# Kernel tuning notes

Measured on AMD Instinct MI355X. Metric: run time of the kernel, lower is better.

## Reference

```python
import jax, jax.numpy as jnp
import numpy as np

EPS = 1e-5

@jax.custom_vjp
def round_ste(x):
    return jnp.round(x)

def _round_fwd(x):
    return jnp.round(x), None

def _round_bwd(_, g):
    return (g,)

round_ste.defvjp(_round_fwd, _round_bwd)


def setup_inputs() -> dict:
    key = jax.random.key(0)
    ks = jax.random.split(key, 4)
    x = jax.random.normal(ks[0], (16, 64, 128, 128), dtype=jnp.float32)
    # small init so conv outputs stay in a sane range
    W = jax.random.normal(ks[1], (128, 64, 3, 3), dtype=jnp.float32) * 0.05
    gamma = jnp.ones((128,), dtype=jnp.float32)
    beta = jnp.zeros((128,), dtype=jnp.float32)
    mean = jax.random.normal(ks[2], (128,), dtype=jnp.float32) * 0.1
    var = jax.random.uniform(ks[3], (128,), dtype=jnp.float32) * 0.5 + 0.5
    # Brevitas QuantReLU default learned max ~6.0 (relu6-like init)
    act_scale = jnp.ones((1,), dtype=jnp.float32) * 6.0
    return {"x": x, "W": W, "gamma": gamma, "beta": beta,
            "mean": mean, "var": var, "act_scale": act_scale}


def reference(x, W, gamma, beta, mean, var, act_scale):
    # --- Int8 per-tensor weight quant-dequant (symmetric, scale = maxabs/127) ---
    w_scale = jnp.max(jnp.abs(W)) / 127.0
    qW = jnp.clip(round_ste(W / w_scale), -127.0, 127.0) * w_scale
    # --- conv2d, stride 1, padding 1, no bias (NCHW / OIHW) ---
    y = jax.lax.conv_general_dilated(
        x, qW, window_strides=(1, 1), padding=[(1, 1), (1, 1)],
        dimension_numbers=("NCHW", "OIHW", "NCHW"))
    # --- BatchNorm (inference form with running stats) ---
    scale = (gamma / jnp.sqrt(var + EPS))[None, :, None, None]
    shift = (beta - gamma * mean / jnp.sqrt(var + EPS))[None, :, None, None]
    y = y * scale + shift
    # --- QuantReLU: relu + uint8 per-tensor quant-dequant ---
    y = jax.nn.relu(y)
    s = act_scale[0] / 255.0
    return jnp.clip(round_ste(y / s), 0.0, 255.0) * s
```

## Files before the change

kernel.cpp:

```cpp
#include <hip/hip_runtime.h>
#include <math.h>

typedef __bf16 bf16x8 __attribute__((ext_vector_type(8)));
typedef float  f32x16 __attribute__((ext_vector_type(16)));
typedef float  f32x4v __attribute__((ext_vector_type(4)));

#define CIN    64
#define KOUT   128
#define HGT    128
#define WID    128
#define NBATCH 16
#define BN_EPS 1e-5f

#define WQ_OFF   256u
#define XT_OFF   (1u << 20)
#define WS_NEED  ((size_t)XT_OFF + (size_t)NBATCH * HGT * WID * CIN * 2)

__global__ __launch_bounds__(256) void wmax_kernel(const float* __restrict__ W,
                                                   unsigned* __restrict__ wsmax) {
    int idx = blockIdx.x * 256 + threadIdx.x;
    const float4* W4 = (const float4*)W;
    float4 v = W4[idx];
    float m = fmaxf(fmaxf(fabsf(v.x), fabsf(v.y)), fmaxf(fabsf(v.z), fabsf(v.w)));
    #pragma unroll
    for (int off = 32; off > 0; off >>= 1)
        m = fmaxf(m, __shfl_xor(m, off));
    __shared__ float red[4];
    if ((threadIdx.x & 63) == 0) red[threadIdx.x >> 6] = m;
    __syncthreads();
    if (threadIdx.x == 0) {
        m = fmaxf(fmaxf(red[0], red[1]), fmaxf(red[2], red[3]));
        atomicMax(wsmax, __float_as_uint(m));
    }
}

__global__ __launch_bounds__(256) void pack_w(const float* __restrict__ W,
                                              const unsigned* __restrict__ wsmax,
                                              __bf16* __restrict__ wqp) {
    int bid = blockIdx.x;
    int tap = bid % 9, cs = bid / 9;
    int t = threadIdx.x;
    int lane = t & 63, mf = t >> 6;
    float ws = __uint_as_float(*wsmax) / 127.0f;
    int kout  = mf * 32 + (lane & 31);
    int cbase = cs * 16 + (lane >> 5) * 8;
    bf16x8 o;
    #pragma unroll
    for (int j = 0; j < 8; ++j) {
        float w = W[(size_t)(kout * 64 + cbase + j) * 9 + tap];
        float q = rintf(w / ws);
        q = fminf(fmaxf(q, -127.f), 127.f);
        o[j] = (__bf16)q;
    }
    *(bf16x8*)(wqp + (((size_t)bid * 4 + mf) * 64 + lane) * 8) = o;
}

__global__ __launch_bounds__(256) void xform(const float* __restrict__ x,
                                             __bf16* __restrict__ xT) {
    __shared__ float t[CIN * 32];
    int bid = blockIdx.x;
    int wt = bid & 3;
    int h  = (bid >> 2) & 127;
    int n  = bid >> 9;
    int w0 = wt * 32;
    int tid = threadIdx.x;
    const float* src = x + ((size_t)n * CIN * HGT + h) * WID + w0;
    int wlane = tid & 31;
    int cbase = tid >> 5;
    #pragma unroll
    for (int it = 0; it < 8; ++it) {
        int c = cbase + it * 8;
        t[c * 32 + (wlane ^ (c & 31))] = src[(size_t)c * HGT * WID + wlane];
    }
    __syncthreads();
    int w = tid >> 3;
    int chunk = tid & 7;
    bf16x8 o;
    #pragma unroll
    for (int j = 0; j < 8; ++j) {
        int c = chunk * 8 + j;
        o[j] = (__bf16)t[c * 32 + (w ^ (c & 31))];
    }
    *(bf16x8*)(xT + (((size_t)n * HGT + h) * WID + w0 + w) * CIN + chunk * 8) = o;
}

__global__ __launch_bounds__(512, 4) void conv_mfma(
    const __bf16* __restrict__ xT, const __bf16* __restrict__ wqp,
    const float* __restrict__ gamma, const float* __restrict__ beta,
    const float* __restrict__ mean, const float* __restrict__ var,
    const float* __restrict__ act_scale, const unsigned* __restrict__ wsmax,
    float* __restrict__ out)
{
    __shared__ uint4 xs[2720];
    __shared__ uint4 wl[2304];
    __shared__ float sc2[KOUT], sh2[KOUT];

    const int bid0 = blockIdx.x;
    const int bid  = (bid0 & 7) * 128 + (bid0 >> 3);
    const int wb = bid & 3, hb = (bid >> 2) & 15, n = bid >> 6;
    const int h0 = hb * 8, w0 = wb * 32;
    const int tid  = threadIdx.x;
    const int lane = tid & 63;
    const int wave = tid >> 6;
    const int wmf = wave & 3;
    const int wr  = wave >> 2;

    const float s_act = act_scale[0] / 255.0f;
    if (tid < KOUT) {
        float ws  = __uint_as_float(*wsmax) / 127.0f;
        float isd = 1.0f / sqrtf(var[tid] + BN_EPS);
        float sc  = ws * gamma[tid] * isd;
        float sh  = beta[tid] - gamma[tid] * mean[tid] * isd;
        sc2[tid] = sc / s_act;
        sh2[tid] = sh / s_act;
    }

    const __bf16* xn = xT + (size_t)n * HGT * WID * CIN;
    for (int it = tid; it < 2720; it += 512) {
        int pl = it >> 3, chunk = it & 7;
        int r = pl / 34, cc = pl - r * 34;
        int gh = h0 - 1 + r, gw = w0 - 1 + cc;
        uint4 v = make_uint4(0u, 0u, 0u, 0u);
        if ((unsigned)gh < HGT && (unsigned)gw < WID)
            v = *(const uint4*)(xn + ((size_t)gh * WID + gw) * CIN + chunk * 8);
        xs[pl * 8 + (chunk ^ (pl & 7))] = v;
    }
    const uint4* wq4 = (const uint4*)wqp;
    for (int i = tid; i < 2304; i += 512)
        wl[i] = wq4[i];
    __syncthreads();

    const int nn = lane & 31;
    const int kh = lane >> 5;

    const char* xsb = (const char*)xs;
    const char* wlb = (const char*)wl;
    const unsigned abase = (unsigned)(wmf * 1024 + lane * 16);
    const int plb = (wr * 4) * 34 + nn;

    f32x16 acc[4];
    #pragma unroll
    for (int b = 0; b < 4; ++b)
        #pragma unroll
        for (int r = 0; r < 16; ++r) acc[b][r] = 0.0f;

    for (int cs = 0; cs < 4; ++cs) {
        if (cs) {
            __syncthreads();
            for (int i = tid; i < 2304; i += 512)
                wl[i] = wq4[(size_t)cs * 2304 + i];
            __syncthreads();
        }
        const int chb = cs * 2 + kh;
        #pragma unroll
        for (int dx = 0; dx < 3; ++dx) {
            bf16x8 A[3];
            #pragma unroll
            for (int dy = 0; dy < 3; ++dy)
                A[dy] = *(const bf16x8*)(wlb + abase + (unsigned)((dy * 3 + dx) * 4096));
            bf16x8 B[6];
            #pragma unroll
            for (int rr = 0; rr < 6; ++rr) {
                const int pl = plb + rr * 34 + dx;
                B[rr] = *(const bf16x8*)(xsb + (pl * 128 + (((pl & 7) ^ chb) * 16)));
            }
            #pragma unroll
            for (int dy = 0; dy < 3; ++dy) {
                #pragma unroll
                for (int nf = 0; nf < 4; ++nf) {
                    acc[nf] = __builtin_amdgcn_mfma_f32_32x32x16_bf16(A[dy], B[nf + dy], acc[nf], 0, 0, 0);
                }
            }
        }
    }

    __syncthreads();
    float* rep = ((float*)xs) + wave * 1024;

    float scr[16], shr[16];
    #pragma unroll
    for (int reg = 0; reg < 16; ++reg) {
        int k = wmf * 32 + 4 * kh + (reg & 3) + 8 * (reg >> 2);
        scr[reg] = sc2[k];
        shr[reg] = sh2[k];
    }

    #pragma unroll
    for (int nf = 0; nf < 4; ++nf) {
        const int hpix = h0 + wr * 4 + nf;
        #pragma unroll
        for (int reg = 0; reg < 16; ++reg) {
            const int kl = 4 * kh + (reg & 3) + 8 * (reg >> 2);
            float t = fmaf(acc[nf][reg], scr[reg], shr[reg]);
            t = fmaxf(t, 0.0f);
            float q = fminf(rintf(t), 255.0f) * s_act;
            rep[kl * 32 + ((((nn >> 2) ^ (kl & 7)) << 2) | (nn & 3))] = q;
        }
        #pragma unroll
        for (int r = 0; r < 4; ++r) {
            const int row = 8 * r + (lane >> 3);
            f32x4v v = *(const f32x4v*)&rep[row * 32 + ((((lane & 7) ^ (row & 7)) << 2))];
            const int k = wmf * 32 + row;
            float* dst = out + (((size_t)n * KOUT + k) * HGT + hpix) * WID
                             + w0 + ((lane & 7) << 2);
            *(f32x4v*)dst = v;
        }
    }
}

#define CB 4
#define TH 8
#define KB 8
__global__ __launch_bounds__(256) void conv_fallback(
    const float* __restrict__ x, const float* __restrict__ W,
    const float* __restrict__ gamma, const float* __restrict__ beta,
    const float* __restrict__ mean, const float* __restrict__ var,
    const float* __restrict__ act_scale, const unsigned* __restrict__ wsmax,
    float* __restrict__ out)
{
    __shared__ float xsf[CB][TH + 2][WID + 2];
    __shared__ float wsh[CB][9][KB];
    const int bid = blockIdx.x;
    const int hg = bid & 15, kg = (bid >> 4) & 15, n = bid >> 8;
    const int h0 = hg * TH, k0 = kg * KB;
    const int tid = threadIdx.x;
    const int tx = tid & 31, ty = tid >> 5;
    float acc[4][KB];
    #pragma unroll
    for (int j = 0; j < 4; ++j)
        #pragma unroll
        for (int kk = 0; kk < KB; ++kk) acc[j][kk] = 0.f;
    const float w_scale = __uint_as_float(*wsmax) / 127.0f;
    const float* xn = x + (size_t)n * CIN * HGT * WID;
    for (int c0 = 0; c0 < CIN; c0 += CB) {
        __syncthreads();
        for (int i = tid; i < CB * (TH + 2) * (WID + 2); i += 256) {
            int cc = i / ((TH + 2) * (WID + 2));
            int r  = i - cc * ((TH + 2) * (WID + 2));
            int yy = r / (WID + 2);
            int xx = r - yy * (WID + 2);
            int gh = h0 - 1 + yy, gw = xx - 1;
            float v = 0.f;
            if ((unsigned)gh < HGT && (unsigned)gw < WID)
                v = xn[(size_t)(c0 + cc) * HGT * WID + gh * WID + gw];
            xsf[cc][yy][xx] = v;
        }
        for (int i = tid; i < CB * 9 * KB; i += 256) {
            int cc = i / (9 * KB);
            int r  = i - cc * (9 * KB);
            int tap = r / KB, kk = r - tap * KB;
            float w = W[(size_t)((k0 + kk) * CIN + (c0 + cc)) * 9 + tap];
            float q = rintf(w / w_scale);
            q = fminf(fmaxf(q, -127.f), 127.f);
            wsh[cc][tap][kk] = q * w_scale;
        }
        __syncthreads();
        #pragma unroll
        for (int cc = 0; cc < CB; ++cc)
            #pragma unroll
            for (int dy = 0; dy < 3; ++dy) {
                float w0a[KB], w1a[KB], w2a[KB];
                #pragma unroll
                for (int kk = 0; kk < KB; ++kk) {
                    w0a[kk] = wsh[cc][dy * 3 + 0][kk];
                    w1a[kk] = wsh[cc][dy * 3 + 1][kk];
                    w2a[kk] = wsh[cc][dy * 3 + 2][kk];
                }
                const float* row = &xsf[cc][ty + dy][0];
                #pragma unroll
                for (int j = 0; j < 4; ++j) {
                    float v0 = row[tx + 32 * j + 0];
                    float v1 = row[tx + 32 * j + 1];
                    float v2 = row[tx + 32 * j + 2];
                    #pragma unroll
                    for (int kk = 0; kk < KB; ++kk) {
                        acc[j][kk] = fmaf(v0, w0a[kk], acc[j][kk]);
                        acc[j][kk] = fmaf(v1, w1a[kk], acc[j][kk]);
                        acc[j][kk] = fmaf(v2, w2a[kk], acc[j][kk]);
                    }
                }
            }
    }
    const float s_act = act_scale[0] / 255.0f;
    const float inv_s = 1.0f / s_act;
    const int h = h0 + ty;
    #pragma unroll
    for (int kk = 0; kk < KB; ++kk) {
        int k = k0 + kk;
        float isd = 1.0f / sqrtf(var[k] + BN_EPS);
        float sc = gamma[k] * isd;
        float sh = beta[k] - gamma[k] * mean[k] * isd;
        float* orow = out + (((size_t)n * KOUT + k) * HGT + h) * WID;
        #pragma unroll
        for (int j = 0; j < 4; ++j) {
            float y = fmaf(acc[j][kk], sc, sh);
            y = fmaxf(y, 0.f);
            float q = rintf(y * inv_s);
            q = fminf(q, 255.f);
            orow[tx + 32 * j] = q * s_act;
        }
    }
}

extern "C" void kernel_launch(void* const* d_in, const int* in_sizes, int n_in,
                              void* d_out, int out_size, void* d_ws, size_t ws_size,
                              hipStream_t stream) {
    const float* x         = (const float*)d_in[0];
    const float* W         = (const float*)d_in[1];
    const float* gamma     = (const float*)d_in[2];
    const float* beta      = (const float*)d_in[3];
    const float* mean      = (const float*)d_in[4];
    const float* var       = (const float*)d_in[5];
    const float* act_scale = (const float*)d_in[6];
    unsigned* wsmax = (unsigned*)d_ws;

    hipMemsetAsync(d_ws, 0, sizeof(unsigned), stream);
    wmax_kernel<<<72, 256, 0, stream>>>(W, wsmax);

    if (ws_size >= WS_NEED) {
        __bf16* wqp = (__bf16*)((char*)d_ws + WQ_OFF);
        __bf16* xT  = (__bf16*)((char*)d_ws + XT_OFF);
        pack_w<<<36, 256, 0, stream>>>(W, wsmax, wqp);
        xform<<<NBATCH * HGT * 4, 256, 0, stream>>>(x, xT);
        conv_mfma<<<NBATCH * 64, 512, 0, stream>>>(
            xT, wqp, gamma, beta, mean, var, act_scale, wsmax, (float*)d_out);
    } else {
        conv_fallback<<<4096, 256, 0, stream>>>(
            x, W, gamma, beta, mean, var, act_scale, wsmax, (float*)d_out);
    }
}
```

Baseline: 88.43 us.

## Double-buffer weight slices in LDS via async global_load_lds per tap column

The weight pack kernel now lays out quantized weights by (channel slice, dx, dy). This lets the conv kernel stream one 12 KB weight slice per (cs, dx) phase into a two-entry LDS ring using global_load_lds, prefetching the next slice while MFMAs run on the current one. It replaces the stop-and-copy reload of the full 36 KB weight block every channel slice, which needed two barriers each time, and it shrinks the LDS footprint. MFMA sections are also wrapped in s_setprio raises. The cost is one barrier per phase, and correctness relies on the async LDS loads having completed by that barrier.

```diff
diff --git a/kernel.cpp b/kernel.cpp
--- a/kernel.cpp
+++ b/kernel.cpp
@@ -39,6 +39,7 @@
                                               __bf16* __restrict__ wqp) {
     int bid = blockIdx.x;
     int tap = bid % 9, cs = bid / 9;
+    int dy = tap / 3, dx = tap % 3;
     int t = threadIdx.x;
     int lane = t & 63, mf = t >> 6;
     float ws = __uint_as_float(*wsmax) / 127.0f;
@@ -52,7 +53,8 @@
         q = fminf(fmaxf(q, -127.f), 127.f);
         o[j] = (__bf16)q;
     }
-    *(bf16x8*)(wqp + (((size_t)bid * 4 + mf) * 64 + lane) * 8) = o;
+    int f = ((cs * 3 + dx) * 3 + dy) * 4 + mf;
+    *(bf16x8*)(wqp + ((size_t)f * 64 + lane) * 8) = o;
 }
 
 __global__ __launch_bounds__(256) void xform(const float* __restrict__ x,
@@ -92,7 +94,7 @@
     float* __restrict__ out)
 {
     __shared__ uint4 xs[2720];
-    __shared__ uint4 wl[2304];
+    __shared__ uint4 wl[2][768];
     __shared__ float sc2[KOUT], sh2[KOUT];
 
     const int bid0 = blockIdx.x;
@@ -105,6 +107,21 @@
     const int wmf = wave & 3;
     const int wr  = wave >> 2;
 
+    const uint4* wq4 = (const uint4*)wqp;
+    #define STAGE(c, buf)                                                          \
+      do {                                                                         \
+        const uint4* _src = wq4 + (size_t)(c) * 768;                               \
+        uint4* _dst = (buf);                                                       \
+        __builtin_amdgcn_global_load_lds((const void*)(_src + wave * 64 + lane),   \
+                                         (void*)(_dst + wave * 64), 16, 0, 0);     \
+        if (wave < 4)                                                              \
+          __builtin_amdgcn_global_load_lds(                                        \
+              (const void*)(_src + (8 + wave) * 64 + lane),                        \
+              (void*)(_dst + (8 + wave) * 64), 16, 0, 0);                          \
+      } while (0)
+
+    STAGE(0, wl[0]);
+
     const float s_act = act_scale[0] / 255.0f;
     if (tid < KOUT) {
         float ws  = __uint_as_float(*wsmax) / 127.0f;
@@ -125,16 +142,12 @@
             v = *(const uint4*)(xn + ((size_t)gh * WID + gw) * CIN + chunk * 8);
         xs[pl * 8 + (chunk ^ (pl & 7))] = v;
     }
-    const uint4* wq4 = (const uint4*)wqp;
-    for (int i = tid; i < 2304; i += 512)
-        wl[i] = wq4[i];
     __syncthreads();
 
     const int nn = lane & 31;
     const int kh = lane >> 5;
 
     const char* xsb = (const char*)xs;
-    const char* wlb = (const char*)wl;
     const unsigned abase = (unsigned)(wmf * 1024 + lane * 16);
     const int plb = (wr * 4) * 34 + nn;
 
@@ -144,37 +157,36 @@
         #pragma unroll
         for (int r = 0; r < 16; ++r) acc[b][r] = 0.0f;
 
-    for (int cs = 0; cs < 4; ++cs) {
-        if (cs) {
-            __syncthreads();
-            for (int i = tid; i < 2304; i += 512)
-                wl[i] = wq4[(size_t)cs * 2304 + i];
-            __syncthreads();
-        }
+    #pragma unroll
+    for (int p = 0; p < 12; ++p) {
+        const int cs = p / 3, dx = p % 3;
+        if (p < 11)
+            STAGE(p + 1, wl[(p + 1) & 1]);
+        const char* wlb = (const char*)wl[p & 1];
+        bf16x8 A[3];
+        #pragma unroll
+        for (int dy = 0; dy < 3; ++dy)
+            A[dy] = *(const bf16x8*)(wlb + abase + (unsigned)(dy * 4096));
         const int chb = cs * 2 + kh;
-        #pragma unroll
-        for (int dx = 0; dx < 3; ++dx) {
-            bf16x8 A[3];
+        bf16x8 B[6];
+        #pragma unroll
+        for (int rr = 0; rr < 6; ++rr) {
+            const int pl = plb + rr * 34 + dx;
+            B[rr] = *(const bf16x8*)(xsb + (pl * 128 + (((pl & 7) ^ chb) * 16)));
+        }
+        __builtin_amdgcn_s_setprio(1);
+        #pragma unroll
+        for (int dy = 0; dy < 3; ++dy) {
             #pragma unroll
-            for (int dy = 0; dy < 3; ++dy)
-                A[dy] = *(const bf16x8*)(wlb + abase + (unsigned)((dy * 3 + dx) * 4096));
-            bf16x8 B[6];
-            #pragma unroll
-            for (int rr = 0; rr < 6; ++rr) {
-                const int pl = plb + rr * 34 + dx;
-                B[rr] = *(const bf16x8*)(xsb + (pl * 128 + (((pl & 7) ^ chb) * 16)));
+            for (int nf = 0; nf < 4; ++nf) {
+                acc[nf] = __builtin_amdgcn_mfma_f32_32x32x16_bf16(A[dy], B[nf + dy], acc[nf], 0, 0, 0);
             }
-            #pragma unroll
-            for (int dy = 0; dy < 3; ++dy) {
-                #pragma unroll
-                for (int nf = 0; nf < 4; ++nf) {
-                    acc[nf] = __builtin_amdgcn_mfma_f32_32x32x16_bf16(A[dy], B[nf + dy], acc[nf], 0, 0, 0);
-                }
-            }
-        }
-    }
-
-    __syncthreads();
+        }
+        __builtin_amdgcn_s_setprio(0);
+        __syncthreads();
+    }
+    #undef STAGE
+
     float* rep = ((float*)xs) + wave * 1024;
 
     float scr[16], shr[16];
```

Result: slower. 101.8 us, median of 2 (+15.1%).

## Fuse NCHW-to-NHWC bf16 transform into conv kernel halo load

Applied to the files above, without the earlier changes.

Removes the separate xform kernel that transposed x to channels-last bf16 in workspace. The conv kernel now reads fp32 NCHW input directly, converts to bf16 and writes the swizzled shared-memory tile itself. This drops a full write and reread of a 32 MB intermediate plus one launch. The cost is that each thread now does eight strided scalar loads per chunk, with neighbouring threads sharing a channel group and walking along width, and the halo rows and columns are reloaded by adjacent blocks.

```diff
diff --git a/kernel.cpp b/kernel.cpp
--- a/kernel.cpp
+++ b/kernel.cpp
@@ -13,8 +13,7 @@
 #define BN_EPS 1e-5f
 
 #define WQ_OFF   256u
-#define XT_OFF   (1u << 20)
-#define WS_NEED  ((size_t)XT_OFF + (size_t)NBATCH * HGT * WID * CIN * 2)
+#define WS_NEED  ((size_t)WQ_OFF + 147456u)
 
 __global__ __launch_bounds__(256) void wmax_kernel(const float* __restrict__ W,
                                                    unsigned* __restrict__ wsmax) {
@@ -53,39 +52,11 @@
         o[j] = (__bf16)q;
     }
     *(bf16x8*)(wqp + (((size_t)bid * 4 + mf) * 64 + lane) * 8) = o;
-}
-
-__global__ __launch_bounds__(256) void xform(const float* __restrict__ x,
-                                             __bf16* __restrict__ xT) {
-    __shared__ float t[CIN * 32];
-    int bid = blockIdx.x;
-    int wt = bid & 3;
-    int h  = (bid >> 2) & 127;
-    int n  = bid >> 9;
-    int w0 = wt * 32;
-    int tid = threadIdx.x;
-    const float* src = x + ((size_t)n * CIN * HGT + h) * WID + w0;
-    int wlane = tid & 31;
-    int cbase = tid >> 5;
-    #pragma unroll
-    for (int it = 0; it < 8; ++it) {
-        int c = cbase + it * 8;
-        t[c * 32 + (wlane ^ (c & 31))] = src[(size_t)c * HGT * WID + wlane];
-    }
-    __syncthreads();
-    int w = tid >> 3;
-    int chunk = tid & 7;
-    bf16x8 o;
-    #pragma unroll
-    for (int j = 0; j < 8; ++j) {
-        int c = chunk * 8 + j;
-        o[j] = (__bf16)t[c * 32 + (w ^ (c & 31))];
-    }
-    *(bf16x8*)(xT + (((size_t)n * HGT + h) * WID + w0 + w) * CIN + chunk * 8) = o;
+    (void)cs;
 }
 
 __global__ __launch_bounds__(512, 4) void conv_mfma(
-    const __bf16* __restrict__ xT, const __bf16* __restrict__ wqp,
+    const float* __restrict__ x, const __bf16* __restrict__ wqp,
     const float* __restrict__ gamma, const float* __restrict__ beta,
     const float* __restrict__ mean, const float* __restrict__ var,
     const float* __restrict__ act_scale, const unsigned* __restrict__ wsmax,
@@ -115,15 +86,24 @@
         sh2[tid] = sh / s_act;
     }
 
-    const __bf16* xn = xT + (size_t)n * HGT * WID * CIN;
-    for (int it = tid; it < 2720; it += 512) {
-        int pl = it >> 3, chunk = it & 7;
+    const float* xnf = x + (size_t)n * CIN * HGT * WID;
+    for (int i = tid; i < 2720; i += 512) {
+        int chunk = i / 340;
+        int pl    = i - chunk * 340;
         int r = pl / 34, cc = pl - r * 34;
         int gh = h0 - 1 + r, gw = w0 - 1 + cc;
-        uint4 v = make_uint4(0u, 0u, 0u, 0u);
-        if ((unsigned)gh < HGT && (unsigned)gw < WID)
-            v = *(const uint4*)(xn + ((size_t)gh * WID + gw) * CIN + chunk * 8);
-        xs[pl * 8 + (chunk ^ (pl & 7))] = v;
+        bf16x8 v;
+        if ((unsigned)gh < HGT && (unsigned)gw < WID) {
+            const float* s = xnf + (size_t)(chunk * 8) * (HGT * WID) + gh * WID + gw;
+            #pragma unroll
+            for (int j = 0; j < 8; ++j)
+                v[j] = (__bf16)s[(size_t)j * (HGT * WID)];
+        } else {
+            #pragma unroll
+            for (int j = 0; j < 8; ++j)
+                v[j] = (__bf16)0.0f;
+        }
+        *(bf16x8*)((char*)xs + (pl * 128 + ((chunk ^ (pl & 7)) * 16))) = v;
     }
     const uint4* wq4 = (const uint4*)wqp;
     for (int i = tid; i < 2304; i += 512)
@@ -319,11 +299,9 @@
 
     if (ws_size >= WS_NEED) {
         __bf16* wqp = (__bf16*)((char*)d_ws + WQ_OFF);
-        __bf16* xT  = (__bf16*)((char*)d_ws + XT_OFF);
         pack_w<<<36, 256, 0, stream>>>(W, wsmax, wqp);
-        xform<<<NBATCH * HGT * 4, 256, 0, stream>>>(x, xT);
         conv_mfma<<<NBATCH * 64, 512, 0, stream>>>(
-            xT, wqp, gamma, beta, mean, var, act_scale, wsmax, (float*)d_out);
+            x, wqp, gamma, beta, mean, var, act_scale, wsmax, (float*)d_out);
     } else {
         conv_fallback<<<4096, 256, 0, stream>>>(
             x, W, gamma, beta, mean, var, act_scale, wsmax, (float*)d_out);
```

After: 78.38 us. 11.4% less time.
